# Performance work log

Measured on AMD Instinct MI355X. Metric: run time of the kernel, lower is better.

## Reference

```python
import jax, jax.numpy as jnp
import numpy as np

D_MODEL = 1024
N_HEADS = 16
HEAD_DIM = D_MODEL // N_HEADS  # 64; used only as softmax scale in windowed path
WINDOW = 128


def _window_starts(seq_len, window):
    # Faithful to the torch loop: stride = window//2, last window right-aligned.
    starts = []
    for i in range(0, seq_len, window // 2):
        end = min(i + window, seq_len)
        starts.append(max(0, end - window))
        if end == seq_len:
            break
    return np.asarray(starts, dtype=np.int32)


def setup_inputs() -> dict:
    key = jax.random.key(0)
    ks = jax.random.split(key, 9)
    B, S = 4, 4096
    sc = 1.0 / np.sqrt(D_MODEL)
    return {
        "x": jax.random.normal(ks[0], (B, S, D_MODEL), jnp.float32),
        "Wq": jax.random.normal(ks[1], (D_MODEL, D_MODEL), jnp.float32) * sc,
        "bq": jax.random.normal(ks[2], (D_MODEL,), jnp.float32) * 0.02,
        "Wk": jax.random.normal(ks[3], (D_MODEL, D_MODEL), jnp.float32) * sc,
        "bk": jax.random.normal(ks[4], (D_MODEL,), jnp.float32) * 0.02,
        "Wv": jax.random.normal(ks[5], (D_MODEL, D_MODEL), jnp.float32) * sc,
        "bv": jax.random.normal(ks[6], (D_MODEL,), jnp.float32) * 0.02,
        "Wo": jax.random.normal(ks[7], (D_MODEL, D_MODEL), jnp.float32) * sc,
        "bo": jax.random.normal(ks[8], (D_MODEL,), jnp.float32) * 0.02,
    }


def reference(x, Wq, bq, Wk, bk, Wv, bv, Wo, bo):
    B, S, D = x.shape
    q = x @ Wq + bq  # [B,S,D]
    k = x @ Wk + bk
    v = x @ Wv + bv

    # Overlapping sliding windows (heads merged, as in the original windowed path).
    starts = _window_starts(S, WINDOW)                      # [W]
    idx = starts[:, None] + np.arange(WINDOW)[None, :]      # [W, w] static
    idx_j = jnp.asarray(idx)
    qw = q[:, idx_j]  # [B, W, w, D]
    kw = k[:, idx_j]
    vw = v[:, idx_j]
    scores = jnp.einsum('bwqd,bwkd->bwqk', qw, kw) / np.sqrt(HEAD_DIM)
    attn = jax.nn.softmax(scores, axis=-1)
    out_w = jnp.einsum('bwqk,bwkd->bwqd', attn, vw)         # [B, W, w, D]

    # Overlap-add then average by coverage counts.
    flat_idx = idx.reshape(-1)
    out = jnp.zeros((B, S, D), x.dtype).at[:, flat_idx].add(
        out_w.reshape(B, -1, D))
    counts = jnp.zeros((S,), x.dtype).at[flat_idx].add(1.0)
    out = out / counts[None, :, None]

    return out @ Wo + bo
```

## Files before the change

kernel.cpp:

```cpp
#include <hip/hip_runtime.h>
#include <stdint.h>
#include <stddef.h>

#define D_MODEL 1024
#define SEQ     4096
#define BATCH   4
#define MTOT    (BATCH*SEQ)
#define NWIN    63

typedef __bf16 bf16;
typedef __bf16 bf16x8 __attribute__((ext_vector_type(8)));
typedef __bf16 bf16x4 __attribute__((ext_vector_type(4)));
typedef float  floatx4 __attribute__((ext_vector_type(4)));

__device__ __forceinline__ void async_ld16(const void* g, void* l) {
  __builtin_amdgcn_global_load_lds(
      (const __attribute__((address_space(1))) unsigned int*)g,
      (__attribute__((address_space(3))) unsigned int*)l,
      16, 0, 0);
}


__global__ __launch_bounds__(256)
void cvt_x_kernel(const float* __restrict__ x, bf16* __restrict__ xb)
{
  const int i = blockIdx.x * 256 + threadIdx.x;
  const float4 v = ((const float4*)x)[i];
  bf16x4 o = { (bf16)v.x, (bf16)v.y, (bf16)v.z, (bf16)v.w };
  ((bf16x4*)xb)[i] = o;
}

__global__ __launch_bounds__(256)
void cvt_wt_kernel(const float* __restrict__ W0, const float* __restrict__ W1,
                   const float* __restrict__ W2, const float* __restrict__ W3,
                   bf16* __restrict__ wt)
{
  __shared__ float tile[32][33];
  const float* Wsel = (blockIdx.z == 0) ? W0 : (blockIdx.z == 1) ? W1
                    : (blockIdx.z == 2) ? W2 : W3;
  bf16* Wt = wt + (size_t)blockIdx.z * D_MODEL * D_MODEL;
  const int tx = threadIdx.x & 31, ty = threadIdx.x >> 5;
  const int tn = blockIdx.x * 32, tk = blockIdx.y * 32;
#pragma unroll
  for (int j = 0; j < 32; j += 8)
    tile[ty + j][tx] = Wsel[(size_t)(tk + ty + j) * D_MODEL + (tn + tx)];
  __syncthreads();
#pragma unroll
  for (int j = 0; j < 32; j += 8)
    Wt[(size_t)(tn + ty + j) * D_MODEL + (tk + tx)] = (bf16)tile[tx][ty + j];
}

template<int SMODE>
__global__ __launch_bounds__(256)
void gemm_bt(const bf16* __restrict__ A, const bf16* __restrict__ Bt,
             const float* __restrict__ bias, void* __restrict__ Cout,
             int Kdim, int Ndim)
{
  __shared__ __attribute__((aligned(16))) bf16 As[8192];
  __shared__ __attribute__((aligned(16))) bf16 Bs[8192];
  const int tid = threadIdx.x;
  const int w  = tid >> 6, l = tid & 63;
  const int ll = l & 15,  lh = l >> 4;
  const int m0 = blockIdx.y * 128, n0 = blockIdx.x * 128;
  const int wm = w >> 1, wn = w & 1;

  floatx4 acc[4][4];
#pragma unroll
  for (int i = 0; i < 4; ++i)
#pragma unroll
    for (int j = 0; j < 4; ++j) acc[i][j] = (floatx4)0.f;

  for (int k0 = 0; k0 < Kdim; k0 += 64) {
#pragma unroll
    for (int i = 0; i < 4; ++i) {
      const int f = w * 4 + i;
      const int mt = f & 7, kk = f >> 3;
      async_ld16(A  + (size_t)(m0 + mt * 16 + ll) * Kdim + (k0 + kk * 32 + lh * 8),
                 &As[f * 512 + l * 8]);
      async_ld16(Bt + (size_t)(n0 + mt * 16 + ll) * Kdim + (k0 + kk * 32 + lh * 8),
                 &Bs[f * 512 + l * 8]);
    }
    __syncthreads();
#pragma unroll
    for (int kk = 0; kk < 2; ++kk) {
      bf16x8 af[4], bfr[4];
#pragma unroll
      for (int t = 0; t < 4; ++t) {
        af[t]  = *(const bf16x8*)&As[(kk * 8 + wm * 4 + t) * 512 + l * 8];
        bfr[t] = *(const bf16x8*)&Bs[(kk * 8 + wn * 4 + t) * 512 + l * 8];
      }
#pragma unroll
      for (int mt = 0; mt < 4; ++mt)
#pragma unroll
        for (int nt = 0; nt < 4; ++nt)
          acc[mt][nt] = __builtin_amdgcn_mfma_f32_16x16x32_bf16(af[mt], bfr[nt], acc[mt][nt], 0, 0, 0);
    }
    __syncthreads();
  }

#pragma unroll
  for (int mt = 0; mt < 4; ++mt) {
#pragma unroll
    for (int nt = 0; nt < 4; ++nt) {
      const int col = n0 + wn * 64 + nt * 16 + ll;
      const float bv = bias[col];
#pragma unroll
      for (int r = 0; r < 4; ++r) {
        const int row = m0 + wm * 64 + mt * 16 + lh * 4 + r;
        const float v = acc[mt][nt][r] + bv;
        if (SMODE == 0) {
          ((bf16*)Cout)[(size_t)row * Ndim + col] = (bf16)v;
        } else if (SMODE == 1) {
          const int bb = row >> 12, s = row & 4095;
          ((bf16*)Cout)[((size_t)bb * D_MODEL + col) * SEQ + s] = (bf16)v;
        } else {
          ((float*)Cout)[(size_t)row * Ndim + col] = v;
        }
      }
    }
  }
}

__global__ __launch_bounds__(256)
void qk_softmax(const bf16* __restrict__ qb, const bf16* __restrict__ kb,
                bf16* __restrict__ Pg)
{
  __shared__ __attribute__((aligned(16))) bf16 As[4096];
  __shared__ __attribute__((aligned(16))) bf16 Bs[8192];
  __shared__ float redM[4][64];
  __shared__ float redS[4][64];

  const int tid = threadIdx.x;
  const int w = tid >> 6, l = tid & 63, ll = l & 15, lh = l >> 4;
  const int wh = blockIdx.x;
  const int win = wh >> 1, half = wh & 1;
  const int b = blockIdx.y;

  const bf16* Aq = qb + ((size_t)b * SEQ + win * 64 + half * 64) * D_MODEL;
  const bf16* Ak = kb + ((size_t)b * SEQ + win * 64) * D_MODEL;

  floatx4 acc[4][2];
#pragma unroll
  for (int i = 0; i < 4; ++i)
#pragma unroll
    for (int j = 0; j < 2; ++j) acc[i][j] = (floatx4)0.f;

  for (int c0 = 0; c0 < D_MODEL; c0 += 64) {
#pragma unroll
    for (int i = 0; i < 2; ++i) {
      const int f = w * 2 + i;
      const int mt = f & 3, kk = f >> 2;
      async_ld16(Aq + (size_t)(mt * 16 + ll) * D_MODEL + (c0 + kk * 32 + lh * 8),
                 &As[f * 512 + l * 8]);
    }
#pragma unroll
    for (int i = 0; i < 4; ++i) {
      const int f = w * 4 + i;
      const int mt = f & 7, kk = f >> 3;
      async_ld16(Ak + (size_t)(mt * 16 + ll) * D_MODEL + (c0 + kk * 32 + lh * 8),
                 &Bs[f * 512 + l * 8]);
    }
    __syncthreads();
#pragma unroll
    for (int kk = 0; kk < 2; ++kk) {
      bf16x8 af[4], bfr[2];
#pragma unroll
      for (int t = 0; t < 4; ++t)
        af[t]  = *(const bf16x8*)&As[(kk * 4 + t) * 512 + l * 8];
#pragma unroll
      for (int t = 0; t < 2; ++t)
        bfr[t] = *(const bf16x8*)&Bs[(kk * 8 + w * 2 + t) * 512 + l * 8];
#pragma unroll
      for (int mt = 0; mt < 4; ++mt)
#pragma unroll
        for (int nt = 0; nt < 2; ++nt)
          acc[mt][nt] = __builtin_amdgcn_mfma_f32_16x16x32_bf16(af[mt], bfr[nt], acc[mt][nt], 0, 0, 0);
    }
    __syncthreads();
  }

#pragma unroll
  for (int mt = 0; mt < 4; ++mt)
#pragma unroll
    for (int nt = 0; nt < 2; ++nt)
#pragma unroll
      for (int r = 0; r < 4; ++r) acc[mt][nt][r] *= 0.125f;

#pragma unroll
  for (int mt = 0; mt < 4; ++mt)
#pragma unroll
    for (int r = 0; r < 4; ++r) {
      float m = fmaxf(acc[mt][0][r], acc[mt][1][r]);
      m = fmaxf(m, __shfl_xor(m, 1));
      m = fmaxf(m, __shfl_xor(m, 2));
      m = fmaxf(m, __shfl_xor(m, 4));
      m = fmaxf(m, __shfl_xor(m, 8));
      if (ll == 0) redM[w][mt * 16 + lh * 4 + r] = m;
    }
  __syncthreads();

#pragma unroll
  for (int mt = 0; mt < 4; ++mt)
#pragma unroll
    for (int r = 0; r < 4; ++r) {
      const int row = mt * 16 + lh * 4 + r;
      const float m = fmaxf(fmaxf(redM[0][row], redM[1][row]),
                            fmaxf(redM[2][row], redM[3][row]));
      const float e0 = __expf(acc[mt][0][r] - m);
      const float e1 = __expf(acc[mt][1][r] - m);
      acc[mt][0][r] = e0; acc[mt][1][r] = e1;
      float s = e0 + e1;
      s += __shfl_xor(s, 1);
      s += __shfl_xor(s, 2);
      s += __shfl_xor(s, 4);
      s += __shfl_xor(s, 8);
      if (ll == 0) redS[w][row] = s;
    }
  __syncthreads();

  bf16* Pb = Pg + ((size_t)(b * NWIN + win) * 128 + half * 64) * 128;
#pragma unroll
  for (int mt = 0; mt < 4; ++mt)
#pragma unroll
    for (int r = 0; r < 4; ++r) {
      const int row = mt * 16 + lh * 4 + r;
      const float inv = 1.f / (redS[0][row] + redS[1][row] + redS[2][row] + redS[3][row]);
#pragma unroll
      for (int nt = 0; nt < 2; ++nt)
        Pb[(size_t)row * 128 + w * 32 + nt * 16 + ll] = (bf16)(acc[mt][nt][r] * inv);
    }
}

__global__ __launch_bounds__(256)
void pv_gather(const bf16* __restrict__ Pg, const bf16* __restrict__ vt,
               bf16* __restrict__ ab)
{
  __shared__ __attribute__((aligned(16))) bf16 As[4096];
  __shared__ __attribute__((aligned(16))) bf16 Bs[8192];

  const int tid = threadIdx.x;
  const int w = tid >> 6, l = tid & 63, ll = l & 15, lh = l >> 4;
  const int d0 = blockIdx.x * 128;
  const int h  = blockIdx.y;
  const int b  = blockIdx.z;

  int wseg[2], roff[2];
  int nseg = 0;
  if (h >= 1)        { wseg[nseg] = h - 1; roff[nseg] = 64; ++nseg; }
  if (h <= NWIN - 1) { wseg[nseg] = h;     roff[nseg] = 0;  ++nseg; }
  const float scale = (nseg == 2) ? 0.5f : 1.0f;

  floatx4 acc[4][2];
#pragma unroll
  for (int i = 0; i < 4; ++i)
#pragma unroll
    for (int j = 0; j < 2; ++j) acc[i][j] = (floatx4)0.f;

  for (int sg = 0; sg < nseg; ++sg) {
    const bf16* Pseg = Pg + ((size_t)(b * NWIN + wseg[sg]) * 128 + roff[sg]) * 128;
    const bf16* Vseg = vt + ((size_t)b * D_MODEL + d0) * SEQ + wseg[sg] * 64;
    for (int c0 = 0; c0 < 128; c0 += 64) {
#pragma unroll
      for (int i = 0; i < 2; ++i) {
        const int f = w * 2 + i;
        const int mt = f & 3, kk = f >> 2;
        async_ld16(Pseg + (size_t)(mt * 16 + ll) * 128 + (c0 + kk * 32 + lh * 8),
                   &As[f * 512 + l * 8]);
      }
#pragma unroll
      for (int i = 0; i < 4; ++i) {
        const int f = w * 4 + i;
        const int mt = f & 7, kk = f >> 3;
        async_ld16(Vseg + (size_t)(mt * 16 + ll) * SEQ + (c0 + kk * 32 + lh * 8),
                   &Bs[f * 512 + l * 8]);
      }
      __syncthreads();
#pragma unroll
      for (int kk = 0; kk < 2; ++kk) {
        bf16x8 af[4], bfr[2];
#pragma unroll
        for (int t = 0; t < 4; ++t)
          af[t]  = *(const bf16x8*)&As[(kk * 4 + t) * 512 + l * 8];
#pragma unroll
        for (int t = 0; t < 2; ++t)
          bfr[t] = *(const bf16x8*)&Bs[(kk * 8 + w * 2 + t) * 512 + l * 8];
#pragma unroll
        for (int mt = 0; mt < 4; ++mt)
#pragma unroll
          for (int nt = 0; nt < 2; ++nt)
            acc[mt][nt] = __builtin_amdgcn_mfma_f32_16x16x32_bf16(af[mt], bfr[nt], acc[mt][nt], 0, 0, 0);
      }
      __syncthreads();
    }
  }

#pragma unroll
  for (int mt = 0; mt < 4; ++mt)
#pragma unroll
    for (int nt = 0; nt < 2; ++nt)
#pragma unroll
      for (int r = 0; r < 4; ++r) {
        const int row = h * 64 + mt * 16 + lh * 4 + r;
        const int col = d0 + w * 32 + nt * 16 + ll;
        ab[((size_t)b * SEQ + row) * D_MODEL + col] = (bf16)(acc[mt][nt][r] * scale);
      }
}

extern "C" void kernel_launch(void* const* d_in, const int* in_sizes, int n_in,
                              void* d_out, int out_size, void* d_ws, size_t ws_size,
                              hipStream_t stream)
{
  (void)in_sizes; (void)n_in; (void)out_size;

  const float* x  = (const float*)d_in[0];
  const float* Wq = (const float*)d_in[1];
  const float* bq = (const float*)d_in[2];
  const float* Wk = (const float*)d_in[3];
  const float* bk = (const float*)d_in[4];
  const float* Wv = (const float*)d_in[5];
  const float* bv = (const float*)d_in[6];
  const float* Wo = (const float*)d_in[7];
  const float* bo = (const float*)d_in[8];

  if (ws_size < (size_t)176160768) return;
  char* ws = (char*)d_ws;
  bf16* xb = (bf16*)(ws);
  bf16* pb = (bf16*)(ws);
  bf16* wt = (bf16*)(ws + 33554432);
  bf16* qb = (bf16*)(ws + 41943040);
  bf16* kb = (bf16*)(ws + 75497472);
  bf16* vt = (bf16*)(ws + 109051904);
  bf16* ab = (bf16*)(ws + 142606336);

  cvt_x_kernel<<<16384, 256, 0, stream>>>(x, xb);
  cvt_wt_kernel<<<dim3(32, 32, 4), 256, 0, stream>>>(Wq, Wk, Wv, Wo, wt);

  gemm_bt<0><<<dim3(8, 128), 256, 0, stream>>>(xb, wt,           bq, qb, D_MODEL, D_MODEL);
  gemm_bt<0><<<dim3(8, 128), 256, 0, stream>>>(xb, wt + 1048576, bk, kb, D_MODEL, D_MODEL);
  gemm_bt<1><<<dim3(8, 128), 256, 0, stream>>>(xb, wt + 2097152, bv, vt, D_MODEL, D_MODEL);

  qk_softmax<<<dim3(126, BATCH), 256, 0, stream>>>(qb, kb, pb);
  pv_gather<<<dim3(8, 64, BATCH), 256, 0, stream>>>(pb, vt, ab);

  gemm_bt<2><<<dim3(8, 128), 256, 0, stream>>>(ab, wt + 3145728, bo, (float*)d_out, D_MODEL, D_MODEL);
}
```

Before: 519.2 us.

## Fuse Q/K/V projections into one GEMM launch with XCD-aware block swizzle

Replaces three separate projection GEMM launches with a single 3072-block kernel that treats the concatenated transposed Wq/Wk/Wv as one N=3072 weight and picks the bias and output layout per column block. Both the fused QKV GEMM and the output GEMM now use a 1D grid remapped so that consecutive M tiles share an XCD, which is meant to improve L2 reuse of A rows and remove launch tails. The cost is some per-block branching in the epilogue; the weights are already contiguous in the workspace, so no extra copies are needed.

```diff
diff --git a/kernel.cpp b/kernel.cpp
--- a/kernel.cpp
+++ b/kernel.cpp
@@ -50,25 +50,15 @@
     Wt[(size_t)(tn + ty + j) * D_MODEL + (tk + tx)] = (bf16)tile[tx][ty + j];
 }
 
-template<int SMODE>
-__global__ __launch_bounds__(256)
-void gemm_bt(const bf16* __restrict__ A, const bf16* __restrict__ Bt,
-             const float* __restrict__ bias, void* __restrict__ Cout,
-             int Kdim, int Ndim)
-{
-  __shared__ __attribute__((aligned(16))) bf16 As[8192];
-  __shared__ __attribute__((aligned(16))) bf16 Bs[8192];
-  const int tid = threadIdx.x;
-  const int w  = tid >> 6, l = tid & 63;
-  const int ll = l & 15,  lh = l >> 4;
-  const int m0 = blockIdx.y * 128, n0 = blockIdx.x * 128;
+__device__ __forceinline__ void gemm_core(const bf16* __restrict__ A,
+                                          const bf16* __restrict__ Bt,
+                                          int Kdim, int m0, int n0,
+                                          bf16* As, bf16* Bs,
+                                          floatx4 (&acc)[4][4],
+                                          int w, int l)
+{
+  const int ll = l & 15, lh = l >> 4;
   const int wm = w >> 1, wn = w & 1;
-
-  floatx4 acc[4][4];
-#pragma unroll
-  for (int i = 0; i < 4; ++i)
-#pragma unroll
-    for (int j = 0; j < 4; ++j) acc[i][j] = (floatx4)0.f;
 
   for (int k0 = 0; k0 < Kdim; k0 += 64) {
 #pragma unroll
@@ -97,25 +87,99 @@
     }
     __syncthreads();
   }
+}
+
+__global__ __launch_bounds__(256)
+void gemm_qkv(const bf16* __restrict__ A, const bf16* __restrict__ Bt,
+              const float* __restrict__ bq, const float* __restrict__ bk,
+              const float* __restrict__ bv,
+              bf16* __restrict__ qo, bf16* __restrict__ ko, bf16* __restrict__ vto)
+{
+  __shared__ __attribute__((aligned(16))) bf16 As[8192];
+  __shared__ __attribute__((aligned(16))) bf16 Bs[8192];
+  const int tid = threadIdx.x;
+  const int w = tid >> 6, l = tid & 63;
+  const int ll = l & 15, lh = l >> 4;
+  const int wm = w >> 1, wn = w & 1;
+
+  const int idx = blockIdx.x;
+  const int xcd = idx & 7;
+  const int local = idx >> 3;
+  const int mblk = xcd * 16 + (local & 15);
+  const int nblk = local >> 4;
+  const int m0 = mblk * 128, n0 = nblk * 128;
+
+  floatx4 acc[4][4];
+#pragma unroll
+  for (int i = 0; i < 4; ++i)
+#pragma unroll
+    for (int j = 0; j < 4; ++j) acc[i][j] = (floatx4)0.f;
+
+  gemm_core(A, Bt, D_MODEL, m0, n0, As, Bs, acc, w, l);
+
+  const int sel = n0 >> 10;
+  const int ncl = n0 & 1023;
+  const float* bias = (sel == 0) ? bq : (sel == 1) ? bk : bv;
+
+#pragma unroll
+  for (int mt = 0; mt < 4; ++mt) {
+#pragma unroll
+    for (int nt = 0; nt < 4; ++nt) {
+      const int colL = ncl + wn * 64 + nt * 16 + ll;
+      const float bvv = bias[colL];
+#pragma unroll
+      for (int r = 0; r < 4; ++r) {
+        const int row = m0 + wm * 64 + mt * 16 + lh * 4 + r;
+        const float v = acc[mt][nt][r] + bvv;
+        if (sel == 0) {
+          qo[(size_t)row * D_MODEL + colL] = (bf16)v;
+        } else if (sel == 1) {
+          ko[(size_t)row * D_MODEL + colL] = (bf16)v;
+        } else {
+          const int bb = row >> 12, s = row & 4095;
+          vto[((size_t)bb * D_MODEL + colL) * SEQ + s] = (bf16)v;
+        }
+      }
+    }
+  }
+}
+
+__global__ __launch_bounds__(256)
+void gemm_out(const bf16* __restrict__ A, const bf16* __restrict__ Bt,
+              const float* __restrict__ bias, float* __restrict__ C)
+{
+  __shared__ __attribute__((aligned(16))) bf16 As[8192];
+  __shared__ __attribute__((aligned(16))) bf16 Bs[8192];
+  const int tid = threadIdx.x;
+  const int w = tid >> 6, l = tid & 63;
+  const int ll = l & 15, lh = l >> 4;
+  const int wm = w >> 1, wn = w & 1;
+
+  const int idx = blockIdx.x;
+  const int xcd = idx & 7;
+  const int local = idx >> 3;
+  const int mblk = xcd * 16 + (local & 15);
+  const int nblk = local >> 4;
+  const int m0 = mblk * 128, n0 = nblk * 128;
+
+  floatx4 acc[4][4];
+#pragma unroll
+  for (int i = 0; i < 4; ++i)
+#pragma unroll
+    for (int j = 0; j < 4; ++j) acc[i][j] = (floatx4)0.f;
+
+  gemm_core(A, Bt, D_MODEL, m0, n0, As, Bs, acc, w, l);
 
 #pragma unroll
   for (int mt = 0; mt < 4; ++mt) {
 #pragma unroll
     for (int nt = 0; nt < 4; ++nt) {
       const int col = n0 + wn * 64 + nt * 16 + ll;
-      const float bv = bias[col];
+      const float bvv = bias[col];
 #pragma unroll
       for (int r = 0; r < 4; ++r) {
         const int row = m0 + wm * 64 + mt * 16 + lh * 4 + r;
-        const float v = acc[mt][nt][r] + bv;
-        if (SMODE == 0) {
-          ((bf16*)Cout)[(size_t)row * Ndim + col] = (bf16)v;
-        } else if (SMODE == 1) {
-          const int bb = row >> 12, s = row & 4095;
-          ((bf16*)Cout)[((size_t)bb * D_MODEL + col) * SEQ + s] = (bf16)v;
-        } else {
-          ((float*)Cout)[(size_t)row * Ndim + col] = v;
-        }
+        C[(size_t)row * D_MODEL + col] = acc[mt][nt][r] + bvv;
       }
     }
   }
@@ -335,12 +399,10 @@
   cvt_x_kernel<<<16384, 256, 0, stream>>>(x, xb);
   cvt_wt_kernel<<<dim3(32, 32, 4), 256, 0, stream>>>(Wq, Wk, Wv, Wo, wt);
 
-  gemm_bt<0><<<dim3(8, 128), 256, 0, stream>>>(xb, wt,           bq, qb, D_MODEL, D_MODEL);
-  gemm_bt<0><<<dim3(8, 128), 256, 0, stream>>>(xb, wt + 1048576, bk, kb, D_MODEL, D_MODEL);
-  gemm_bt<1><<<dim3(8, 128), 256, 0, stream>>>(xb, wt + 2097152, bv, vt, D_MODEL, D_MODEL);
+  gemm_qkv<<<3072, 256, 0, stream>>>(xb, wt, bq, bk, bv, qb, kb, vt);
 
   qk_softmax<<<dim3(126, BATCH), 256, 0, stream>>>(qb, kb, pb);
   pv_gather<<<dim3(8, 64, BATCH), 256, 0, stream>>>(pb, vt, ab);
 
-  gemm_bt<2><<<dim3(8, 128), 256, 0, stream>>>(ab, wt + 3145728, bo, (float*)d_out, D_MODEL, D_MODEL);
-}
+  gemm_out<<<1024, 256, 0, stream>>>(ab, wt + 3145728, bo, (float*)d_out);
+}
```

Measured after the change: 498.6 us. 1.04x faster.
